# Optimization experiments

Hardware: AMD Instinct MI355X
Metric: run time of the kernel (lower is better)

The kernel has to match this reference:

```python
import jax, jax.numpy as jnp
import numpy as np

# Ground-plane grid from proj_2DTo2D: W = 640/4 = 160, H = 480/4 = 120
GP_H, GP_W = 120, 160
PATCH_NUM = 1


def setup_inputs() -> dict:
    key = jax.random.key(0)
    k1, k2, k3 = jax.random.split(key, 3)
    nR, fh, fw, fdim = 4, 90, 160, 512  # 4 camera views, quarter-res feature maps
    nV = GP_H * GP_W  # 19200 ground-plane points per view
    inputs = jax.random.normal(k1, (nR, fh, fw, fdim), dtype=jnp.float32)
    # Projected image-plane coordinates (stand-in for calibration-based World2Image)
    im_x = jax.random.uniform(k2, (nR, nV), dtype=jnp.float32) * (fw - 1)
    im_y = jax.random.uniform(k3, (nR, nV), dtype=jnp.float32) * (fh - 1)
    return {"inputs": inputs, "im_x": im_x, "im_y": im_y}


def reference(inputs, im_x, im_y):
    # inputs: [nR, fh, fw, fdim]; im_x/im_y: [nR, nV] float pixel coords
    nR, fh, fw, fdim = inputs.shape
    im_x = jnp.clip(im_x, 0.0, fw - 1)
    im_y = jnp.clip(im_y, 0.0, fh - 1)
    x0 = jnp.floor(im_x).astype(jnp.int32)
    x1 = jnp.clip(x0 + 1, 0, fw - 1)
    y0 = jnp.floor(im_y).astype(jnp.int32)
    y1 = jnp.clip(y0 + 1, 0, fh - 1)
    x0f, x1f = x0.astype(im_x.dtype), x1.astype(im_x.dtype)
    y0f, y1f = y0.astype(im_y.dtype), y1.astype(im_y.dtype)

    b = jnp.arange(nR)[:, None]  # [nR, 1] batch index per grid point
    Ia = inputs[b, y0, x0]  # [nR, nV, fdim]
    Ib = inputs[b, y1, x0]
    Ic = inputs[b, y0, x1]
    Id = inputs[b, y1, x1]

    wa = ((x1f - im_x) * (y1f - im_y))[..., None]
    wb = ((x1f - im_x) * (im_y - y0f))[..., None]
    wc = ((im_x - x0f) * (y1f - im_y))[..., None]
    wd = ((im_x - x0f) * (im_y - y0f))[..., None]

    Ibilin = wa * Ia + wb * Ib + wc * Ic + wd * Id  # [nR, nV, fdim]
    return Ibilin.reshape(nR // PATCH_NUM, PATCH_NUM, GP_H, GP_W, fdim)
```

## Files before the change

### kernel.cpp

```cpp
#include <hip/hip_runtime.h>


typedef float f32x4 __attribute__((ext_vector_type(4)));

#define GLOBAL_AS __attribute__((address_space(1)))
#define LDS_AS    __attribute__((address_space(3)))

constexpr int NR   = 4;
constexpr int FH   = 90;
constexpr int FW   = 160;
constexpr int FDIM = 512;
constexpr int NV   = 120 * 160;
constexpr int NPTS = NR * NV;
constexpr int C4   = FDIM / 4;

constexpr int BY   = 3;
constexpr int BX   = 5;
constexpr int NGY  = FH / BY;
constexpr int NGX  = FW / BX;
constexpr int NBINS = NR * NGY * NGX;
constexpr int SY   = BY + 1;
constexpr int SX   = BX + 1;
constexpr int SCELLS = SY * SX;

constexpr int CAP   = 48;
constexpr int OVCAP = 4096;
constexpr int TPB   = 512;

__global__ void k_zero(int* __restrict__ cnts) {
    int i = blockIdx.x * blockDim.x + threadIdx.x;
    if (i < NBINS + 1) cnts[i] = 0;
}

__global__ void k_scatter(const float* __restrict__ imx, const float* __restrict__ imy,
                          int* __restrict__ binCnt, int* __restrict__ ovCnt,
                          int* __restrict__ perm, float* __restrict__ sX,
                          float* __restrict__ sY, int* __restrict__ ovList) {
    int pt = blockIdx.x * blockDim.x + threadIdx.x;
    if (pt >= NPTS) return;
    int r = pt / NV;
    float x = imx[pt], y = imy[pt];
    x = fminf(fmaxf(x, 0.0f), (float)(FW - 1));
    y = fminf(fmaxf(y, 0.0f), (float)(FH - 1));
    int x0 = (int)floorf(x);
    int y0 = (int)floorf(y);
    int b = (r * NGY + y0 / BY) * NGX + x0 / BX;
    int slot = atomicAdd(&binCnt[b], 1);
    if (slot < CAP) {
        int idx = b * CAP + slot;
        perm[idx] = pt;
        sX[idx] = x;
        sY[idx] = y;
    } else {
        int o = atomicAdd(ovCnt, 1);
        if (o < OVCAP) ovList[o] = pt;
    }
}

__device__ __forceinline__ f32x4 lerp4(f32x4 A, f32x4 B, f32x4 C, f32x4 D,
                                       float wa, float wb, float wc, float wd) {
    return wa * A + wb * B + wc * C + wd * D;
}

__device__ __forceinline__ void weights_and_cells(float x, float y,
                                                  int& x0, int& x1, int& y0, int& y1,
                                                  float& wa, float& wb, float& wc, float& wd) {
    float x0f = floorf(x), y0f = floorf(y);
    x0 = (int)x0f; y0 = (int)y0f;
    x1 = min(x0 + 1, FW - 1);
    y1 = min(y0 + 1, FH - 1);
    float wx1 = (float)x1 - x;
    float wx0 = x - x0f;
    float wy1 = (float)y1 - y;
    float wy0 = y - y0f;
    wa = wx1 * wy1; wb = wx1 * wy0; wc = wx0 * wy1; wd = wx0 * wy0;
}

__global__ __launch_bounds__(TPB) void st_bins(
    const float* __restrict__ inp,
    const int* __restrict__ binCnt,
    const int* __restrict__ ovCnt,
    const int* __restrict__ perm,
    const float* __restrict__ sX,
    const float* __restrict__ sY,
    const int* __restrict__ ovList,
    const float* __restrict__ imx,
    const float* __restrict__ imy,
    float* __restrict__ out)
{
    __shared__ f32x4 lds[SCELLS * C4];
    __shared__ int   pmS[CAP];
    __shared__ float pxS[CAP];
    __shared__ float pyS[CAP];

    int p = blockIdx.x;
    int b = (p & 7) * (NBINS >> 3) + (p >> 3);

    int r   = b / (NGY * NGX);
    int by0 = (b / NGX % NGY) * BY;
    int bx0 = (b % NGX) * BX;
    int tid = threadIdx.x;

    const f32x4* in4 = (const f32x4*)inp;
    int cnt  = min(binCnt[b], CAP);
    int base = b * CAP;

    #pragma unroll
    for (int i = 0; i < (SCELLS * C4) / TPB; ++i) {
        int idx  = tid + i * TPB;
        int cell = idx >> 7;
        int c4   = idx & (C4 - 1);
        int ry   = cell / SX;
        int rx   = cell - ry * SX;
        int gy   = min(by0 + ry, FH - 1);
        int gx   = min(bx0 + rx, FW - 1);
        const void* gsrc = (const void*)(in4 + (size_t)((r * FH + gy) * FW + gx) * C4 + c4);
        __builtin_amdgcn_global_load_lds(
            (const GLOBAL_AS void*)gsrc,
            (LDS_AS void*)&lds[idx], 16, 0, 0);
    }
    if (tid < cnt) {
        pmS[tid] = perm[base + tid];
        pxS[tid] = sX[base + tid];
        pyS[tid] = sY[base + tid];
    }
    __syncthreads();

    int g  = tid >> 7;
    int c4 = tid & (C4 - 1);
    f32x4* out4 = (f32x4*)out;

    int i = g;
    for (; i + 4 < cnt; i += 8) {
        int   ptA = pmS[i];
        float xA  = pxS[i], yA = pyS[i];
        int   ptB = pmS[i + 4];
        float xB  = pxS[i + 4], yB = pyS[i + 4];

        int x0A, x1A, y0A, y1A, x0B, x1B, y0B, y1B;
        float waA, wbA, wcA, wdA, waB, wbB, wcB, wdB;
        weights_and_cells(xA, yA, x0A, x1A, y0A, y1A, waA, wbA, wcA, wdA);
        weights_and_cells(xB, yB, x0B, x1B, y0B, y1B, waB, wbB, wcB, wdB);

        f32x4 Aa = lds[(((y0A - by0) * SX + (x0A - bx0)) << 7) + c4];
        f32x4 Ab = lds[(((y1A - by0) * SX + (x0A - bx0)) << 7) + c4];
        f32x4 Ac = lds[(((y0A - by0) * SX + (x1A - bx0)) << 7) + c4];
        f32x4 Ad = lds[(((y1A - by0) * SX + (x1A - bx0)) << 7) + c4];
        f32x4 Ba = lds[(((y0B - by0) * SX + (x0B - bx0)) << 7) + c4];
        f32x4 Bb = lds[(((y1B - by0) * SX + (x0B - bx0)) << 7) + c4];
        f32x4 Bc = lds[(((y0B - by0) * SX + (x1B - bx0)) << 7) + c4];
        f32x4 Bd = lds[(((y1B - by0) * SX + (x1B - bx0)) << 7) + c4];

        __builtin_nontemporal_store(lerp4(Aa, Ab, Ac, Ad, waA, wbA, wcA, wdA),
                                    out4 + (size_t)ptA * C4 + c4);
        __builtin_nontemporal_store(lerp4(Ba, Bb, Bc, Bd, waB, wbB, wcB, wdB),
                                    out4 + (size_t)ptB * C4 + c4);
    }
    if (i < cnt) {
        int   pt = pmS[i];
        float x  = pxS[i], y = pyS[i];
        int x0, x1, y0, y1; float wa, wb, wc, wd;
        weights_and_cells(x, y, x0, x1, y0, y1, wa, wb, wc, wd);
        f32x4 A = lds[(((y0 - by0) * SX + (x0 - bx0)) << 7) + c4];
        f32x4 B = lds[(((y1 - by0) * SX + (x0 - bx0)) << 7) + c4];
        f32x4 C = lds[(((y0 - by0) * SX + (x1 - bx0)) << 7) + c4];
        f32x4 D = lds[(((y1 - by0) * SX + (x1 - bx0)) << 7) + c4];
        __builtin_nontemporal_store(lerp4(A, B, C, D, wa, wb, wc, wd),
                                    out4 + (size_t)pt * C4 + c4);
    }

    int ov = min(*ovCnt, OVCAP);
    for (int j = b; j < ov; j += NBINS) {
        if (g != 0) continue;
        int pt = ovList[j];
        int rr = pt / NV;
        float x = imx[pt], y = imy[pt];
        x = fminf(fmaxf(x, 0.0f), (float)(FW - 1));
        y = fminf(fmaxf(y, 0.0f), (float)(FH - 1));
        int x0, x1, y0, y1; float wa, wb, wc, wd;
        weights_and_cells(x, y, x0, x1, y0, y1, wa, wb, wc, wd);
        int rb = rr * FH;
        f32x4 A = in4[(size_t)((rb + y0) * FW + x0) * C4 + c4];
        f32x4 B = in4[(size_t)((rb + y1) * FW + x0) * C4 + c4];
        f32x4 C = in4[(size_t)((rb + y0) * FW + x1) * C4 + c4];
        f32x4 D = in4[(size_t)((rb + y1) * FW + x1) * C4 + c4];
        __builtin_nontemporal_store(lerp4(A, B, C, D, wa, wb, wc, wd),
                                    out4 + (size_t)pt * C4 + c4);
    }
}

__global__ __launch_bounds__(256) void st_bilinear_direct(
    const float* __restrict__ inp,
    const float* __restrict__ imx,
    const float* __restrict__ imy,
    float* __restrict__ out)
{
    int gid = blockIdx.x * blockDim.x + threadIdx.x;
    int pt = gid >> 7;
    int c4 = gid & (C4 - 1);
    if (pt >= NPTS) return;
    int r = pt / NV;
    float x = imx[pt], y = imy[pt];
    x = fminf(fmaxf(x, 0.0f), (float)(FW - 1));
    y = fminf(fmaxf(y, 0.0f), (float)(FH - 1));
    int x0, x1, y0, y1; float wa, wb, wc, wd;
    weights_and_cells(x, y, x0, x1, y0, y1, wa, wb, wc, wd);
    const f32x4* base = (const f32x4*)inp;
    int rb = r * FH;
    f32x4 a = base[(size_t)((rb + y0) * FW + x0) * C4 + c4];
    f32x4 b = base[(size_t)((rb + y1) * FW + x0) * C4 + c4];
    f32x4 c = base[(size_t)((rb + y0) * FW + x1) * C4 + c4];
    f32x4 d = base[(size_t)((rb + y1) * FW + x1) * C4 + c4];
    ((f32x4*)out)[(size_t)pt * C4 + c4] = lerp4(a, b, c, d, wa, wb, wc, wd);
}

extern "C" void kernel_launch(void* const* d_in, const int* in_sizes, int n_in,
                              void* d_out, int out_size, void* d_ws, size_t ws_size,
                              hipStream_t stream) {
    const float* inp = (const float*)d_in[0];
    const float* imx = (const float*)d_in[1];
    const float* imy = (const float*)d_in[2];
    float* out = (float*)d_out;

    size_t nInts = (size_t)NBINS + 1 + (size_t)NBINS * CAP * 3 + OVCAP;
    size_t need  = nInts * sizeof(int);

    if (ws_size < need) {
        int nblocks = (NPTS * C4) / 256;
        hipLaunchKernelGGL(st_bilinear_direct, dim3(nblocks), dim3(256), 0, stream,
                           inp, imx, imy, out);
        return;
    }

    int*   binCnt = (int*)d_ws;
    int*   ovCnt  = binCnt + NBINS;
    int*   perm   = ovCnt + 1;
    float* sX     = (float*)(perm + NBINS * CAP);
    float* sY     = sX + NBINS * CAP;
    int*   ovList = (int*)(sY + NBINS * CAP);

    hipLaunchKernelGGL(k_zero, dim3((NBINS + 1 + 255) / 256), dim3(256), 0, stream,
                       binCnt);
    hipLaunchKernelGGL(k_scatter, dim3((NPTS + 255) / 256), dim3(256), 0, stream,
                       imx, imy, binCnt, ovCnt, perm, sX, sY, ovList);
    hipLaunchKernelGGL(st_bins, dim3(NBINS), dim3(TPB), 0, stream,
                       inp, binCnt, ovCnt, perm, sX, sY, ovList, imx, imy, out);
}
```

Before: 58.87 us.

## Make bin kernel persistent with double-buffered LDS staging across bins

The bin kernel now launches 256 persistent blocks instead of one block per bin. Each block walks 15 consecutive bins and prefetches the next bin's feature cells into a second LDS buffer with global_load_lds while it interpolates the current one, using explicit waitcnt and barriers to keep the two buffers apart. Point coordinates are packed as float2, and the zeroing kernel is replaced by hipMemsetAsync. The goal is to overlap feature loads with compute and cut per-block launch and staging overhead. The cost is about 105KB of LDS per block, so a CU holds at most one 512-thread block and fewer waves are available to hide the latency of the heavy output stores.

After: 62.99 us. 7.0% more time.

```diff
diff --git a/kernel.cpp b/kernel.cpp
--- a/kernel.cpp
+++ b/kernel.cpp
@@ -26,31 +26,25 @@
 constexpr int CAP   = 48;
 constexpr int OVCAP = 4096;
 constexpr int TPB   = 512;
-
-__global__ void k_zero(int* __restrict__ cnts) {
-    int i = blockIdx.x * blockDim.x + threadIdx.x;
-    if (i < NBINS + 1) cnts[i] = 0;
-}
+constexpr int NBLK  = 256;
+constexpr int BPB   = NBINS / NBLK;
+constexpr int LDSX4 = SCELLS * C4;
 
 __global__ void k_scatter(const float* __restrict__ imx, const float* __restrict__ imy,
                           int* __restrict__ binCnt, int* __restrict__ ovCnt,
-                          int* __restrict__ perm, float* __restrict__ sX,
-                          float* __restrict__ sY, int* __restrict__ ovList) {
+                          int* __restrict__ perm, float2* __restrict__ sXY,
+                          int* __restrict__ ovList) {
     int pt = blockIdx.x * blockDim.x + threadIdx.x;
     if (pt >= NPTS) return;
     int r = pt / NV;
-    float x = imx[pt], y = imy[pt];
-    x = fminf(fmaxf(x, 0.0f), (float)(FW - 1));
-    y = fminf(fmaxf(y, 0.0f), (float)(FH - 1));
-    int x0 = (int)floorf(x);
-    int y0 = (int)floorf(y);
-    int b = (r * NGY + y0 / BY) * NGX + x0 / BX;
+    float x = fminf(fmaxf(imx[pt], 0.0f), (float)(FW - 1));
+    float y = fminf(fmaxf(imy[pt], 0.0f), (float)(FH - 1));
+    int b = (r * NGY + (int)floorf(y) / BY) * NGX + (int)floorf(x) / BX;
     int slot = atomicAdd(&binCnt[b], 1);
     if (slot < CAP) {
         int idx = b * CAP + slot;
         perm[idx] = pt;
-        sX[idx] = x;
-        sY[idx] = y;
+        sXY[idx] = make_float2(x, y);
     } else {
         int o = atomicAdd(ovCnt, 1);
         if (o < OVCAP) ovList[o] = pt;
@@ -76,37 +70,13 @@
     wa = wx1 * wy1; wb = wx1 * wy0; wc = wx0 * wy1; wd = wx0 * wy0;
 }
 
-__global__ __launch_bounds__(TPB) void st_bins(
-    const float* __restrict__ inp,
-    const int* __restrict__ binCnt,
-    const int* __restrict__ ovCnt,
-    const int* __restrict__ perm,
-    const float* __restrict__ sX,
-    const float* __restrict__ sY,
-    const int* __restrict__ ovList,
-    const float* __restrict__ imx,
-    const float* __restrict__ imy,
-    float* __restrict__ out)
-{
-    __shared__ f32x4 lds[SCELLS * C4];
-    __shared__ int   pmS[CAP];
-    __shared__ float pxS[CAP];
-    __shared__ float pyS[CAP];
-
-    int p = blockIdx.x;
-    int b = (p & 7) * (NBINS >> 3) + (p >> 3);
-
+__device__ __forceinline__ void stage_bin(const f32x4* __restrict__ in4,
+                                          f32x4* ldsbuf, int b, int tid) {
     int r   = b / (NGY * NGX);
     int by0 = (b / NGX % NGY) * BY;
     int bx0 = (b % NGX) * BX;
-    int tid = threadIdx.x;
-
-    const f32x4* in4 = (const f32x4*)inp;
-    int cnt  = min(binCnt[b], CAP);
-    int base = b * CAP;
-
     #pragma unroll
-    for (int i = 0; i < (SCELLS * C4) / TPB; ++i) {
+    for (int i = 0; i < LDSX4 / TPB; ++i) {
         int idx  = tid + i * TPB;
         int cell = idx >> 7;
         int c4   = idx & (C4 - 1);
@@ -114,69 +84,120 @@
         int rx   = cell - ry * SX;
         int gy   = min(by0 + ry, FH - 1);
         int gx   = min(bx0 + rx, FW - 1);
-        const void* gsrc = (const void*)(in4 + (size_t)((r * FH + gy) * FW + gx) * C4 + c4);
         __builtin_amdgcn_global_load_lds(
-            (const GLOBAL_AS void*)gsrc,
-            (LDS_AS void*)&lds[idx], 16, 0, 0);
-    }
-    if (tid < cnt) {
-        pmS[tid] = perm[base + tid];
-        pxS[tid] = sX[base + tid];
-        pyS[tid] = sY[base + tid];
-    }
-    __syncthreads();
+            (const GLOBAL_AS void*)(in4 + (size_t)((r * FH + gy) * FW + gx) * C4 + c4),
+            (LDS_AS void*)&ldsbuf[idx], 16, 0, 0);
+    }
+}
+
+__global__ __launch_bounds__(TPB) void st_bins(
+    const float* __restrict__ inp,
+    const int* __restrict__ binCnt,
+    const int* __restrict__ ovCnt,
+    const int* __restrict__ perm,
+    const float2* __restrict__ sXY,
+    const int* __restrict__ ovList,
+    const float* __restrict__ imx,
+    const float* __restrict__ imy,
+    float* __restrict__ out)
+{
+    __shared__ f32x4  lds[2 * LDSX4];
+    __shared__ int    pmS[BPB * CAP];
+    __shared__ float2 xyS[BPB * CAP];
+    __shared__ int    cntS[BPB];
+
+    int p   = blockIdx.x;
+    int xcd = p & 7, slot = p >> 3;
+    int l0  = xcd * (NBINS / 8) + slot * BPB;
+
+    int tid = threadIdx.x;
+    const f32x4* in4 = (const f32x4*)inp;
+
+    int mbase = l0 * CAP;
+    for (int i = tid; i < BPB * CAP; i += TPB) {
+        pmS[i] = perm[mbase + i];
+        xyS[i] = sXY[mbase + i];
+    }
+    if (tid < BPB) cntS[tid] = min(binCnt[l0 + tid], CAP);
+    stage_bin(in4, &lds[0], l0, tid);
 
     int g  = tid >> 7;
     int c4 = tid & (C4 - 1);
     f32x4* out4 = (f32x4*)out;
-
-    int i = g;
-    for (; i + 4 < cnt; i += 8) {
-        int   ptA = pmS[i];
-        float xA  = pxS[i], yA = pyS[i];
-        int   ptB = pmS[i + 4];
-        float xB  = pxS[i + 4], yB = pyS[i + 4];
-
-        int x0A, x1A, y0A, y1A, x0B, x1B, y0B, y1B;
-        float waA, wbA, wcA, wdA, waB, wbB, wcB, wdB;
-        weights_and_cells(xA, yA, x0A, x1A, y0A, y1A, waA, wbA, wcA, wdA);
-        weights_and_cells(xB, yB, x0B, x1B, y0B, y1B, waB, wbB, wcB, wdB);
-
-        f32x4 Aa = lds[(((y0A - by0) * SX + (x0A - bx0)) << 7) + c4];
-        f32x4 Ab = lds[(((y1A - by0) * SX + (x0A - bx0)) << 7) + c4];
-        f32x4 Ac = lds[(((y0A - by0) * SX + (x1A - bx0)) << 7) + c4];
-        f32x4 Ad = lds[(((y1A - by0) * SX + (x1A - bx0)) << 7) + c4];
-        f32x4 Ba = lds[(((y0B - by0) * SX + (x0B - bx0)) << 7) + c4];
-        f32x4 Bb = lds[(((y1B - by0) * SX + (x0B - bx0)) << 7) + c4];
-        f32x4 Bc = lds[(((y0B - by0) * SX + (x1B - bx0)) << 7) + c4];
-        f32x4 Bd = lds[(((y1B - by0) * SX + (x1B - bx0)) << 7) + c4];
-
-        __builtin_nontemporal_store(lerp4(Aa, Ab, Ac, Ad, waA, wbA, wcA, wdA),
-                                    out4 + (size_t)ptA * C4 + c4);
-        __builtin_nontemporal_store(lerp4(Ba, Bb, Bc, Bd, waB, wbB, wcB, wdB),
-                                    out4 + (size_t)ptB * C4 + c4);
-    }
-    if (i < cnt) {
-        int   pt = pmS[i];
-        float x  = pxS[i], y = pyS[i];
-        int x0, x1, y0, y1; float wa, wb, wc, wd;
-        weights_and_cells(x, y, x0, x1, y0, y1, wa, wb, wc, wd);
-        f32x4 A = lds[(((y0 - by0) * SX + (x0 - bx0)) << 7) + c4];
-        f32x4 B = lds[(((y1 - by0) * SX + (x0 - bx0)) << 7) + c4];
-        f32x4 C = lds[(((y0 - by0) * SX + (x1 - bx0)) << 7) + c4];
-        f32x4 D = lds[(((y1 - by0) * SX + (x1 - bx0)) << 7) + c4];
-        __builtin_nontemporal_store(lerp4(A, B, C, D, wa, wb, wc, wd),
-                                    out4 + (size_t)pt * C4 + c4);
+    int cur = 0;
+
+    for (int k = 0; k < BPB; ++k) {
+        int b = l0 + k;
+        if (k + 1 < BPB)
+            stage_bin(in4, &lds[(cur ^ 1) * LDSX4], b + 1, tid);
+
+        if (k + 1 < BPB)
+            asm volatile("s_waitcnt vmcnt(6) lgkmcnt(0)" ::: "memory");
+        else
+            asm volatile("s_waitcnt vmcnt(0) lgkmcnt(0)" ::: "memory");
+        __builtin_amdgcn_sched_barrier(0);
+        __builtin_amdgcn_s_barrier();
+        __builtin_amdgcn_sched_barrier(0);
+
+        {
+            const f32x4* buf = &lds[cur * LDSX4];
+            int by0 = (b / NGX % NGY) * BY;
+            int bx0 = (b % NGX) * BX;
+            int cnt  = cntS[k];
+            int mofs = k * CAP;
+
+            int i = g;
+            for (; i + 4 < cnt; i += 8) {
+                int    ptA = pmS[mofs + i];
+                float2 cA  = xyS[mofs + i];
+                int    ptB = pmS[mofs + i + 4];
+                float2 cB  = xyS[mofs + i + 4];
+
+                int x0A, x1A, y0A, y1A, x0B, x1B, y0B, y1B;
+                float waA, wbA, wcA, wdA, waB, wbB, wcB, wdB;
+                weights_and_cells(cA.x, cA.y, x0A, x1A, y0A, y1A, waA, wbA, wcA, wdA);
+                weights_and_cells(cB.x, cB.y, x0B, x1B, y0B, y1B, waB, wbB, wcB, wdB);
+
+                f32x4 Aa = buf[(((y0A - by0) * SX + (x0A - bx0)) << 7) + c4];
+                f32x4 Ab = buf[(((y1A - by0) * SX + (x0A - bx0)) << 7) + c4];
+                f32x4 Ac = buf[(((y0A - by0) * SX + (x1A - bx0)) << 7) + c4];
+                f32x4 Ad = buf[(((y1A - by0) * SX + (x1A - bx0)) << 7) + c4];
+                f32x4 Ba = buf[(((y0B - by0) * SX + (x0B - bx0)) << 7) + c4];
+                f32x4 Bb = buf[(((y1B - by0) * SX + (x0B - bx0)) << 7) + c4];
+                f32x4 Bc = buf[(((y0B - by0) * SX + (x1B - bx0)) << 7) + c4];
+                f32x4 Bd = buf[(((y1B - by0) * SX + (x1B - bx0)) << 7) + c4];
+
+                __builtin_nontemporal_store(lerp4(Aa, Ab, Ac, Ad, waA, wbA, wcA, wdA),
+                                            out4 + (size_t)ptA * C4 + c4);
+                __builtin_nontemporal_store(lerp4(Ba, Bb, Bc, Bd, waB, wbB, wcB, wdB),
+                                            out4 + (size_t)ptB * C4 + c4);
+            }
+            if (i < cnt) {
+                int    pt = pmS[mofs + i];
+                float2 cc = xyS[mofs + i];
+                int x0, x1, y0, y1; float wa, wb, wc, wd;
+                weights_and_cells(cc.x, cc.y, x0, x1, y0, y1, wa, wb, wc, wd);
+                f32x4 A = buf[(((y0 - by0) * SX + (x0 - bx0)) << 7) + c4];
+                f32x4 B = buf[(((y1 - by0) * SX + (x0 - bx0)) << 7) + c4];
+                f32x4 C = buf[(((y0 - by0) * SX + (x1 - bx0)) << 7) + c4];
+                f32x4 D = buf[(((y1 - by0) * SX + (x1 - bx0)) << 7) + c4];
+                __builtin_nontemporal_store(lerp4(A, B, C, D, wa, wb, wc, wd),
+                                            out4 + (size_t)pt * C4 + c4);
+            }
+        }
+
+        __builtin_amdgcn_sched_barrier(0);
+        __builtin_amdgcn_s_barrier();
+        cur ^= 1;
     }
 
     int ov = min(*ovCnt, OVCAP);
-    for (int j = b; j < ov; j += NBINS) {
+    for (int j = p; j < ov; j += NBLK) {
         if (g != 0) continue;
         int pt = ovList[j];
         int rr = pt / NV;
-        float x = imx[pt], y = imy[pt];
-        x = fminf(fmaxf(x, 0.0f), (float)(FW - 1));
-        y = fminf(fmaxf(y, 0.0f), (float)(FH - 1));
+        float x = fminf(fmaxf(imx[pt], 0.0f), (float)(FW - 1));
+        float y = fminf(fmaxf(imy[pt], 0.0f), (float)(FH - 1));
         int x0, x1, y0, y1; float wa, wb, wc, wd;
         weights_and_cells(x, y, x0, x1, y0, y1, wa, wb, wc, wd);
         int rb = rr * FH;
@@ -200,9 +221,8 @@
     int c4 = gid & (C4 - 1);
     if (pt >= NPTS) return;
     int r = pt / NV;
-    float x = imx[pt], y = imy[pt];
-    x = fminf(fmaxf(x, 0.0f), (float)(FW - 1));
-    y = fminf(fmaxf(y, 0.0f), (float)(FH - 1));
+    float x = fminf(fmaxf(imx[pt], 0.0f), (float)(FW - 1));
+    float y = fminf(fmaxf(imy[pt], 0.0f), (float)(FH - 1));
     int x0, x1, y0, y1; float wa, wb, wc, wd;
     weights_and_cells(x, y, x0, x1, y0, y1, wa, wb, wc, wd);
     const f32x4* base = (const f32x4*)inp;
@@ -222,8 +242,8 @@
     const float* imy = (const float*)d_in[2];
     float* out = (float*)d_out;
 
-    size_t nInts = (size_t)NBINS + 1 + (size_t)NBINS * CAP * 3 + OVCAP;
-    size_t need  = nInts * sizeof(int);
+    size_t need = (size_t)(NBINS + 1 + NBINS * CAP + OVCAP) * sizeof(int)
+                + (size_t)NBINS * CAP * sizeof(float2);
 
     if (ws_size < need) {
         int nblocks = (NPTS * C4) / 256;
@@ -232,17 +252,15 @@
         return;
     }
 
-    int*   binCnt = (int*)d_ws;
-    int*   ovCnt  = binCnt + NBINS;
-    int*   perm   = ovCnt + 1;
-    float* sX     = (float*)(perm + NBINS * CAP);
-    float* sY     = sX + NBINS * CAP;
-    int*   ovList = (int*)(sY + NBINS * CAP);
-
-    hipLaunchKernelGGL(k_zero, dim3((NBINS + 1 + 255) / 256), dim3(256), 0, stream,
-                       binCnt);
+    int*    binCnt = (int*)d_ws;
+    int*    ovCnt  = binCnt + NBINS;
+    int*    perm   = ovCnt + 1;
+    float2* sXY    = (float2*)(perm + (size_t)NBINS * CAP);
+    int*    ovList = (int*)(sXY + (size_t)NBINS * CAP);
+
+    hipMemsetAsync(binCnt, 0, (NBINS + 1) * sizeof(int), stream);
     hipLaunchKernelGGL(k_scatter, dim3((NPTS + 255) / 256), dim3(256), 0, stream,
-                       imx, imy, binCnt, ovCnt, perm, sX, sY, ovList);
-    hipLaunchKernelGGL(st_bins, dim3(NBINS), dim3(TPB), 0, stream,
-                       inp, binCnt, ovCnt, perm, sX, sY, ovList, imx, imy, out);
-}
+                       imx, imy, binCnt, ovCnt, perm, sXY, ovList);
+    hipLaunchKernelGGL(st_bins, dim3(NBLK), dim3(TPB), 0, stream,
+                       inp, binCnt, ovCnt, perm, sXY, ovList, imx, imy, out);
+}
```

## Shrink spatial bins, pack bin coordinates as float2, replace zero kernel with memset

Applied to the files above, without the earlier changes.

Bin height drops from three to two rows and per-bin capacity from 48 to 32. Each block therefore stages fewer feature cells in LDS (18 instead of 24), which uses less shared memory per block and gives more, smaller blocks. The per-point x and y coordinates are stored as one interleaved float2 array, so each point needs one load instead of two, and the separate zeroing kernel becomes a hipMemsetAsync. The trade-off is more redundant input-cell loads, since neighbouring bins overlap by a larger fraction. The float2 workspace array also starts at a 4-byte-aligned rather than 8-byte-aligned offset.

Result: no change. 58.60 us (-0.5%).

```diff
diff --git a/kernel.cpp b/kernel.cpp
--- a/kernel.cpp
+++ b/kernel.cpp
@@ -14,7 +14,7 @@
 constexpr int NPTS = NR * NV;
 constexpr int C4   = FDIM / 4;
 
-constexpr int BY   = 3;
+constexpr int BY   = 2;
 constexpr int BX   = 5;
 constexpr int NGY  = FH / BY;
 constexpr int NGX  = FW / BX;
@@ -22,35 +22,27 @@
 constexpr int SY   = BY + 1;
 constexpr int SX   = BX + 1;
 constexpr int SCELLS = SY * SX;
-
-constexpr int CAP   = 48;
+constexpr int LDSX4 = SCELLS * C4;
+
+constexpr int CAP   = 32;
 constexpr int OVCAP = 4096;
 constexpr int TPB   = 512;
 
-__global__ void k_zero(int* __restrict__ cnts) {
-    int i = blockIdx.x * blockDim.x + threadIdx.x;
-    if (i < NBINS + 1) cnts[i] = 0;
-}
-
 __global__ void k_scatter(const float* __restrict__ imx, const float* __restrict__ imy,
                           int* __restrict__ binCnt, int* __restrict__ ovCnt,
-                          int* __restrict__ perm, float* __restrict__ sX,
-                          float* __restrict__ sY, int* __restrict__ ovList) {
+                          int* __restrict__ perm, float2* __restrict__ sXY,
+                          int* __restrict__ ovList) {
     int pt = blockIdx.x * blockDim.x + threadIdx.x;
     if (pt >= NPTS) return;
     int r = pt / NV;
-    float x = imx[pt], y = imy[pt];
-    x = fminf(fmaxf(x, 0.0f), (float)(FW - 1));
-    y = fminf(fmaxf(y, 0.0f), (float)(FH - 1));
-    int x0 = (int)floorf(x);
-    int y0 = (int)floorf(y);
-    int b = (r * NGY + y0 / BY) * NGX + x0 / BX;
+    float x = fminf(fmaxf(imx[pt], 0.0f), (float)(FW - 1));
+    float y = fminf(fmaxf(imy[pt], 0.0f), (float)(FH - 1));
+    int b = (r * NGY + (int)floorf(y) / BY) * NGX + (int)floorf(x) / BX;
     int slot = atomicAdd(&binCnt[b], 1);
     if (slot < CAP) {
         int idx = b * CAP + slot;
         perm[idx] = pt;
-        sX[idx] = x;
-        sY[idx] = y;
+        sXY[idx] = make_float2(x, y);
     } else {
         int o = atomicAdd(ovCnt, 1);
         if (o < OVCAP) ovList[o] = pt;
@@ -81,17 +73,15 @@
     const int* __restrict__ binCnt,
     const int* __restrict__ ovCnt,
     const int* __restrict__ perm,
-    const float* __restrict__ sX,
-    const float* __restrict__ sY,
+    const float2* __restrict__ sXY,
     const int* __restrict__ ovList,
     const float* __restrict__ imx,
     const float* __restrict__ imy,
     float* __restrict__ out)
 {
-    __shared__ f32x4 lds[SCELLS * C4];
-    __shared__ int   pmS[CAP];
-    __shared__ float pxS[CAP];
-    __shared__ float pyS[CAP];
+    __shared__ f32x4  lds[LDSX4];
+    __shared__ int    pmS[CAP];
+    __shared__ float2 xyS[CAP];
 
     int p = blockIdx.x;
     int b = (p & 7) * (NBINS >> 3) + (p >> 3);
@@ -106,23 +96,23 @@
     int base = b * CAP;
 
     #pragma unroll
-    for (int i = 0; i < (SCELLS * C4) / TPB; ++i) {
-        int idx  = tid + i * TPB;
-        int cell = idx >> 7;
-        int c4   = idx & (C4 - 1);
-        int ry   = cell / SX;
-        int rx   = cell - ry * SX;
-        int gy   = min(by0 + ry, FH - 1);
-        int gx   = min(bx0 + rx, FW - 1);
-        const void* gsrc = (const void*)(in4 + (size_t)((r * FH + gy) * FW + gx) * C4 + c4);
-        __builtin_amdgcn_global_load_lds(
-            (const GLOBAL_AS void*)gsrc,
-            (LDS_AS void*)&lds[idx], 16, 0, 0);
+    for (int i = 0; i < 5; ++i) {
+        int idx = tid + i * TPB;
+        if (idx < LDSX4) {
+            int cell = idx >> 7;
+            int c4   = idx & (C4 - 1);
+            int ry   = cell / SX;
+            int rx   = cell - ry * SX;
+            int gy   = min(by0 + ry, FH - 1);
+            int gx   = min(bx0 + rx, FW - 1);
+            __builtin_amdgcn_global_load_lds(
+                (const GLOBAL_AS void*)(in4 + (size_t)((r * FH + gy) * FW + gx) * C4 + c4),
+                (LDS_AS void*)&lds[idx], 16, 0, 0);
+        }
     }
     if (tid < cnt) {
         pmS[tid] = perm[base + tid];
-        pxS[tid] = sX[base + tid];
-        pyS[tid] = sY[base + tid];
+        xyS[tid] = sXY[base + tid];
     }
     __syncthreads();
 
@@ -132,15 +122,15 @@
 
     int i = g;
     for (; i + 4 < cnt; i += 8) {
-        int   ptA = pmS[i];
-        float xA  = pxS[i], yA = pyS[i];
-        int   ptB = pmS[i + 4];
-        float xB  = pxS[i + 4], yB = pyS[i + 4];
+        int    ptA = pmS[i];
+        float2 cA  = xyS[i];
+        int    ptB = pmS[i + 4];
+        float2 cB  = xyS[i + 4];
 
         int x0A, x1A, y0A, y1A, x0B, x1B, y0B, y1B;
         float waA, wbA, wcA, wdA, waB, wbB, wcB, wdB;
-        weights_and_cells(xA, yA, x0A, x1A, y0A, y1A, waA, wbA, wcA, wdA);
-        weights_and_cells(xB, yB, x0B, x1B, y0B, y1B, waB, wbB, wcB, wdB);
+        weights_and_cells(cA.x, cA.y, x0A, x1A, y0A, y1A, waA, wbA, wcA, wdA);
+        weights_and_cells(cB.x, cB.y, x0B, x1B, y0B, y1B, waB, wbB, wcB, wdB);
 
         f32x4 Aa = lds[(((y0A - by0) * SX + (x0A - bx0)) << 7) + c4];
         f32x4 Ab = lds[(((y1A - by0) * SX + (x0A - bx0)) << 7) + c4];
@@ -157,10 +147,10 @@
                                     out4 + (size_t)ptB * C4 + c4);
     }
     if (i < cnt) {
-        int   pt = pmS[i];
-        float x  = pxS[i], y = pyS[i];
+        int    pt = pmS[i];
+        float2 cc = xyS[i];
         int x0, x1, y0, y1; float wa, wb, wc, wd;
-        weights_and_cells(x, y, x0, x1, y0, y1, wa, wb, wc, wd);
+        weights_and_cells(cc.x, cc.y, x0, x1, y0, y1, wa, wb, wc, wd);
         f32x4 A = lds[(((y0 - by0) * SX + (x0 - bx0)) << 7) + c4];
         f32x4 B = lds[(((y1 - by0) * SX + (x0 - bx0)) << 7) + c4];
         f32x4 C = lds[(((y0 - by0) * SX + (x1 - bx0)) << 7) + c4];
@@ -174,9 +164,8 @@
         if (g != 0) continue;
         int pt = ovList[j];
         int rr = pt / NV;
-        float x = imx[pt], y = imy[pt];
-        x = fminf(fmaxf(x, 0.0f), (float)(FW - 1));
-        y = fminf(fmaxf(y, 0.0f), (float)(FH - 1));
+        float x = fminf(fmaxf(imx[pt], 0.0f), (float)(FW - 1));
+        float y = fminf(fmaxf(imy[pt], 0.0f), (float)(FH - 1));
         int x0, x1, y0, y1; float wa, wb, wc, wd;
         weights_and_cells(x, y, x0, x1, y0, y1, wa, wb, wc, wd);
         int rb = rr * FH;
@@ -200,9 +189,8 @@
     int c4 = gid & (C4 - 1);
     if (pt >= NPTS) return;
     int r = pt / NV;
-    float x = imx[pt], y = imy[pt];
-    x = fminf(fmaxf(x, 0.0f), (float)(FW - 1));
-    y = fminf(fmaxf(y, 0.0f), (float)(FH - 1));
+    float x = fminf(fmaxf(imx[pt], 0.0f), (float)(FW - 1));
+    float y = fminf(fmaxf(imy[pt], 0.0f), (float)(FH - 1));
     int x0, x1, y0, y1; float wa, wb, wc, wd;
     weights_and_cells(x, y, x0, x1, y0, y1, wa, wb, wc, wd);
     const f32x4* base = (const f32x4*)inp;
@@ -222,8 +210,8 @@
     const float* imy = (const float*)d_in[2];
     float* out = (float*)d_out;
 
-    size_t nInts = (size_t)NBINS + 1 + (size_t)NBINS * CAP * 3 + OVCAP;
-    size_t need  = nInts * sizeof(int);
+    size_t need = (size_t)(NBINS + 1 + NBINS * CAP + OVCAP) * sizeof(int)
+                + (size_t)NBINS * CAP * sizeof(float2);
 
     if (ws_size < need) {
         int nblocks = (NPTS * C4) / 256;
@@ -232,17 +220,15 @@
         return;
     }
 
-    int*   binCnt = (int*)d_ws;
-    int*   ovCnt  = binCnt + NBINS;
-    int*   perm   = ovCnt + 1;
-    float* sX     = (float*)(perm + NBINS * CAP);
-    float* sY     = sX + NBINS * CAP;
-    int*   ovList = (int*)(sY + NBINS * CAP);
-
-    hipLaunchKernelGGL(k_zero, dim3((NBINS + 1 + 255) / 256), dim3(256), 0, stream,
-                       binCnt);
+    int*    binCnt = (int*)d_ws;
+    int*    ovCnt  = binCnt + NBINS;
+    int*    perm   = ovCnt + 1;
+    float2* sXY    = (float2*)(perm + (size_t)NBINS * CAP);
+    int*    ovList = (int*)(sXY + (size_t)NBINS * CAP);
+
+    hipMemsetAsync(binCnt, 0, (NBINS + 1) * sizeof(int), stream);
     hipLaunchKernelGGL(k_scatter, dim3((NPTS + 255) / 256), dim3(256), 0, stream,
-                       imx, imy, binCnt, ovCnt, perm, sX, sY, ovList);
+                       imx, imy, binCnt, ovCnt, perm, sXY, ovList);
     hipLaunchKernelGGL(st_bins, dim3(NBINS), dim3(TPB), 0, stream,
-                       inp, binCnt, ovCnt, perm, sX, sY, ovList, imx, imy, out);
-}
+                       inp, binCnt, ovCnt, perm, sXY, ovList, imx, imy, out);
+}
```
